# Kernel tuning notes

Hardware: AMD Instinct MI355X
Metric: run time of the kernel (lower is better)

The kernel has to match this reference:

```python
import jax, jax.numpy as jnp
import numpy as np

D_EMB = 256
SCALE = 0.02
B, T = 4, 4096
EPS = 1e-5


def layer_norm(x, w, b):
    m = jnp.mean(x, axis=-1, keepdims=True)
    v = jnp.mean((x - m) ** 2, axis=-1, keepdims=True)
    return (x - m) * jax.lax.rsqrt(v + EPS) * w + b


def setup_inputs() -> dict:
    key = jax.random.key(0)
    ks = jax.random.split(key, 4)
    x = jax.random.normal(ks[0], (B, T, D_EMB), dtype=jnp.float32)
    qkv = jax.random.normal(ks[1], (3, D_EMB, D_EMB), dtype=jnp.float32) * SCALE
    # nn.Linear(D, 2D, bias=False): weight shape (2D, D), applied as x @ W.T
    w1 = jax.random.normal(ks[2], (2 * D_EMB, D_EMB), dtype=jnp.float32) * (1.0 / np.sqrt(D_EMB))
    w2 = jax.random.normal(ks[3], (D_EMB, 2 * D_EMB), dtype=jnp.float32) * (1.0 / np.sqrt(2 * D_EMB))
    ones = jnp.ones((D_EMB,), dtype=jnp.float32)
    zeros = jnp.zeros((D_EMB,), dtype=jnp.float32)
    return {
        "x": x, "qkv": qkv,
        "ln_q_w": ones, "ln_q_b": zeros,
        "ln_k_w": ones, "ln_k_b": zeros,
        "ln_attn_w": ones, "ln_attn_b": zeros,
        "w1": w1, "w2": w2,
        "ln_ff_w": ones, "ln_ff_b": zeros,
    }


def reference(x, qkv, ln_q_w, ln_q_b, ln_k_w, ln_k_b, ln_attn_w, ln_attn_b, w1, w2, ln_ff_w, ln_ff_b):
    # QKV projections: [3, B, T, D]
    y = jnp.einsum('btd,ndD->nbtD', x, qkv)
    q, k, v = y[0], y[1], y[2]
    q = layer_norm(q, ln_q_w, ln_q_b)
    k = layer_norm(k, ln_k_w, ln_k_b)
    # full (non-causal) single-head attention, scale by sqrt(D_EMB)
    scores = jnp.einsum('btd,bsd->bts', q, k) / jnp.sqrt(jnp.float32(D_EMB))
    attn = jax.nn.softmax(scores, axis=-1)
    y = jnp.einsum('bts,bsd->btd', attn, v)
    y = layer_norm(y, ln_attn_w, ln_attn_b)
    x = 0.7 * (x + y)
    # FFN with dual leaky_relu
    y = jax.nn.leaky_relu(x @ w1.T, negative_slope=0.2)
    y = jax.nn.leaky_relu(y @ w2.T, negative_slope=0.2)
    y = layer_norm(y, ln_ff_w, ln_ff_b)
    return 0.7 * (x + y)
```

## Files before the change

### kernel.cpp

```cpp
#include <hip/hip_runtime.h>

#define BSZ   4
#define TSEQ  4096
#define DEMB  256
#define NTOK  (BSZ * TSEQ)
#define HID   512
#define SPLITS 4
#define KEYS_PER_SPLIT (TSEQ / SPLITS)
#define TK 32
#define NT (KEYS_PER_SPLIT / TK)
#define KIMG_STRIDE 8704
#define VIMG_STRIDE 10240

using bf16x8 = __attribute__((ext_vector_type(8))) short;
using f32x16 = __attribute__((ext_vector_type(16))) float;

static __device__ __forceinline__ unsigned short f2bf(float f) {
  union { float f; unsigned u; } v; v.f = f;
  unsigned r = v.u + 0x7FFF + ((v.u >> 16) & 1);
  return (unsigned short)(r >> 16);
}
static __device__ __forceinline__ float bf2f(unsigned short u) {
  union { unsigned u; float f; } v; v.u = ((unsigned)u) << 16;
  return v.f;
}

static __device__ __forceinline__ void async16(void* lds, const void* gp) {
  __builtin_amdgcn_global_load_lds(
      (const __attribute__((address_space(1))) unsigned int*)gp,
      (__attribute__((address_space(3))) unsigned int*)lds, 16, 0, 0);
}

__global__ __launch_bounds__(256) void prep_kernel(
    const float* __restrict__ qkv, const float* __restrict__ w1,
    const float* __restrict__ w2, unsigned short* __restrict__ qkvT,
    unsigned short* __restrict__ w1b, unsigned short* __restrict__ w2b)
{
  const int tid = threadIdx.x;
  if (blockIdx.y < 3) {
    if (blockIdx.x >= 16) return;
    __shared__ float Ts[64][65];
    const int z  = blockIdx.y;
    const int k0 = (blockIdx.x >> 2) * 64;
    const int j0 = (blockIdx.x & 3) * 64;
    const float* src = qkv + (size_t)z * DEMB * DEMB + (size_t)k0 * DEMB + j0;
#pragma unroll
    for (int p = 0; p < 4; ++p) {
      int idx = p * 256 + tid;
      int r = idx >> 4, g = idx & 15;
      float4 v = *(const float4*)(src + (size_t)r * DEMB + g * 4);
      Ts[r][g * 4 + 0] = v.x; Ts[r][g * 4 + 1] = v.y;
      Ts[r][g * 4 + 2] = v.z; Ts[r][g * 4 + 3] = v.w;
    }
    __syncthreads();
    unsigned short* dst = qkvT + (size_t)z * DEMB * DEMB + (size_t)j0 * DEMB + k0;
#pragma unroll
    for (int p = 0; p < 4; ++p) {
      int idx = p * 256 + tid;
      int r = idx >> 4, g = idx & 15;
      ushort4 o;
      o.x = f2bf(Ts[g * 4 + 0][r]); o.y = f2bf(Ts[g * 4 + 1][r]);
      o.z = f2bf(Ts[g * 4 + 2][r]); o.w = f2bf(Ts[g * 4 + 3][r]);
      *(ushort4*)(dst + (size_t)r * DEMB + g * 4) = o;
    }
  } else {
    const float* s = (blockIdx.y == 3) ? w1 : w2;
    unsigned short* d = (blockIdx.y == 3) ? w1b : w2b;
    const int i = blockIdx.x * 256 + tid;
    float4 v = ((const float4*)s)[i];
    ushort4 o;
    o.x = f2bf(v.x); o.y = f2bf(v.y); o.z = f2bf(v.z); o.w = f2bf(v.w);
    ((ushort4*)d)[i] = o;
  }
}

template <int ACT, int MODE, int AF32>
__global__ __launch_bounds__(256, 3) void gemm_bf16_kernel(
    const void* __restrict__ Av, const unsigned short* __restrict__ Bt,
    float* __restrict__ Cf, unsigned short* __restrict__ C0,
    unsigned short* __restrict__ C1, unsigned short* __restrict__ C2,
    int M, int N, int K)
{
  __shared__ __align__(16) unsigned short As[128 * 72];
  __shared__ __align__(16) unsigned short Bs[128 * 72];

  const int tid = threadIdx.x;
  const int w   = tid >> 6;
  const int wm  = w >> 1, wn = w & 1;
  const int l   = tid & 63;
  const int lm  = l & 31;
  const int lh  = l >> 5;

  const int m0    = blockIdx.x * 128;
  const int nbase = blockIdx.y * 128;

  f32x16 acc00, acc01, acc10, acc11;
#pragma unroll
  for (int r = 0; r < 16; ++r) { acc00[r] = 0.f; acc01[r] = 0.f; acc10[r] = 0.f; acc11[r] = 0.f; }

  const int lr = tid >> 3;
  const int lc = (tid & 7) * 8;
  const int fr = tid >> 4;
  const int fc = (tid & 15) * 4;

  const unsigned short* Ab = (const unsigned short*)Av;
  const float* Af = (const float*)Av;

  bf16x8 arb[4], brb[4];
  float4 arf[8];

#pragma unroll
  for (int i = 0; i < (AF32 ? 8 : 4); ++i) {
    if (AF32) arf[i] = *(const float4*)(Af + (size_t)(m0 + i * 16 + fr) * K + fc);
    else      arb[i] = *(const bf16x8*)(Ab + (size_t)(m0 + i * 32 + lr) * K + lc);
  }
#pragma unroll
  for (int i = 0; i < 4; ++i)
    brb[i] = *(const bf16x8*)(Bt + (size_t)(nbase + i * 32 + lr) * K + lc);

  for (int k0 = 0; k0 < K; k0 += 64) {
    __syncthreads();
    if (AF32) {
#pragma unroll
      for (int i = 0; i < 8; ++i) {
        ushort4 u;
        u.x = f2bf(arf[i].x); u.y = f2bf(arf[i].y);
        u.z = f2bf(arf[i].z); u.w = f2bf(arf[i].w);
        *(ushort4*)&As[(i * 16 + fr) * 72 + fc] = u;
      }
    } else {
#pragma unroll
      for (int i = 0; i < 4; ++i) *(bf16x8*)&As[(i * 32 + lr) * 72 + lc] = arb[i];
    }
#pragma unroll
    for (int i = 0; i < 4; ++i) *(bf16x8*)&Bs[(i * 32 + lr) * 72 + lc] = brb[i];
    __syncthreads();

    if (k0 + 64 < K) {
      const int kn = k0 + 64;
#pragma unroll
      for (int i = 0; i < (AF32 ? 8 : 4); ++i) {
        if (AF32) arf[i] = *(const float4*)(Af + (size_t)(m0 + i * 16 + fr) * K + kn + fc);
        else      arb[i] = *(const bf16x8*)(Ab + (size_t)(m0 + i * 32 + lr) * K + kn + lc);
      }
#pragma unroll
      for (int i = 0; i < 4; ++i)
        brb[i] = *(const bf16x8*)(Bt + (size_t)(nbase + i * 32 + lr) * K + kn + lc);
    }

#pragma unroll
    for (int ks = 0; ks < 4; ++ks) {
      bf16x8 a0 = *(const bf16x8*)&As[(wm * 64 + lm)      * 72 + ks * 16 + lh * 8];
      bf16x8 a1 = *(const bf16x8*)&As[(wm * 64 + 32 + lm) * 72 + ks * 16 + lh * 8];
      bf16x8 b0 = *(const bf16x8*)&Bs[(wn * 64 + lm)      * 72 + ks * 16 + lh * 8];
      bf16x8 b1 = *(const bf16x8*)&Bs[(wn * 64 + 32 + lm) * 72 + ks * 16 + lh * 8];
      acc00 = __builtin_amdgcn_mfma_f32_32x32x16_bf16(a0, b0, acc00, 0, 0, 0);
      acc01 = __builtin_amdgcn_mfma_f32_32x32x16_bf16(a0, b1, acc01, 0, 0, 0);
      acc10 = __builtin_amdgcn_mfma_f32_32x32x16_bf16(a1, b0, acc10, 0, 0, 0);
      acc11 = __builtin_amdgcn_mfma_f32_32x32x16_bf16(a1, b1, acc11, 0, 0, 0);
    }
  }

  unsigned short* Cb = C0;
  int col0, ldc;
  if (MODE == 2) {
    const int sel = blockIdx.y >> 1;
    Cb = (sel == 0) ? C0 : (sel == 1 ? C1 : C2);
    col0 = (blockIdx.y & 1) * 128;
    ldc = DEMB;
  } else {
    col0 = nbase;
    ldc = N;
  }
  const f32x16* accs[4] = { &acc00, &acc01, &acc10, &acc11 };
#pragma unroll
  for (int am = 0; am < 2; ++am)
#pragma unroll
    for (int bn = 0; bn < 2; ++bn) {
      const f32x16& a = *accs[am * 2 + bn];
#pragma unroll
      for (int r = 0; r < 16; ++r) {
        const int m = m0 + wm * 64 + am * 32 + (r & 3) + 8 * (r >> 2) + 4 * lh;
        const int n = col0 + wn * 64 + bn * 32 + lm;
        float v = a[r];
        if (ACT == 1) v = v > 0.f ? v : 0.2f * v;
        if (MODE == 0) Cf[(size_t)m * ldc + n] = v;
        else           Cb[(size_t)m * ldc + n] = f2bf(v);
      }
    }
}

__global__ __launch_bounds__(256) void ln_qk_kernel(
    const unsigned short* __restrict__ Qraw, const unsigned short* __restrict__ Kraw,
    const float* __restrict__ qw, const float* __restrict__ qb,
    const float* __restrict__ kw, const float* __restrict__ kb,
    unsigned short* __restrict__ Qbn, unsigned short* __restrict__ Kimg)
{
  const int isK = blockIdx.y;
  const unsigned short* X = isK ? Kraw : Qraw;
  const float* w = isK ? kw : qw;
  const float* b = isK ? kb : qb;
  const int lane = threadIdx.x & 63;
  const size_t row = (size_t)blockIdx.x * 4 + (threadIdx.x >> 6);
  ushort4 u = *(const ushort4*)&X[row * DEMB + lane * 4];
  float x0 = bf2f(u.x), x1 = bf2f(u.y), x2 = bf2f(u.z), x3 = bf2f(u.w);
  float s  = x0 + x1 + x2 + x3;
  float sq = x0 * x0 + x1 * x1 + x2 * x2 + x3 * x3;
#pragma unroll
  for (int o = 32; o > 0; o >>= 1) { s += __shfl_down(s, o); sq += __shfl_down(sq, o); }
  s = __shfl(s, 0); sq = __shfl(sq, 0);
  const float m  = s * (1.f / DEMB);
  const float rs = rsqrtf(sq * (1.f / DEMB) - m * m + 1e-5f);
  const float4 wv = *(const float4*)&w[lane * 4];
  const float4 bv = *(const float4*)&b[lane * 4];
  ushort4 o;
  o.x = f2bf((x0 - m) * rs * wv.x + bv.x);
  o.y = f2bf((x1 - m) * rs * wv.y + bv.y);
  o.z = f2bf((x2 - m) * rs * wv.z + bv.z);
  o.w = f2bf((x3 - m) * rs * wv.w + bv.w);
  if (!isK) {
    *(ushort4*)&Qbn[row * DEMB + lane * 4] = o;
  } else {
    const int bb = (int)(row >> 12);
    const int t  = (int)(row & 4095);
    *(ushort4*)&Kimg[(size_t)(bb * 128 + (t >> 5)) * KIMG_STRIDE + (t & 31) * 264 + lane * 4] = o;
  }
}

__global__ __launch_bounds__(256) void ln_res_bf16_kernel(
    const unsigned short* __restrict__ Y, const float* __restrict__ Xin,
    const float* __restrict__ w, const float* __restrict__ b,
    float* __restrict__ Out)
{
  const int lane = threadIdx.x & 63;
  const size_t row = (size_t)blockIdx.x * 4 + (threadIdx.x >> 6);
  ushort4 u = *(const ushort4*)&Y[row * DEMB + lane * 4];
  float y0 = bf2f(u.x), y1 = bf2f(u.y), y2 = bf2f(u.z), y3 = bf2f(u.w);
  float s  = y0 + y1 + y2 + y3;
  float sq = y0 * y0 + y1 * y1 + y2 * y2 + y3 * y3;
#pragma unroll
  for (int o = 32; o > 0; o >>= 1) { s += __shfl_down(s, o); sq += __shfl_down(sq, o); }
  s = __shfl(s, 0); sq = __shfl(sq, 0);
  const float m  = s * (1.f / DEMB);
  const float rs = rsqrtf(sq * (1.f / DEMB) - m * m + 1e-5f);
  const float4 wv = *(const float4*)&w[lane * 4];
  const float4 bv = *(const float4*)&b[lane * 4];
  const float4 xi = *(const float4*)&Xin[row * DEMB + lane * 4];
  float4 o;
  o.x = 0.7f * (xi.x + (y0 - m) * rs * wv.x + bv.x);
  o.y = 0.7f * (xi.y + (y1 - m) * rs * wv.y + bv.y);
  o.z = 0.7f * (xi.z + (y2 - m) * rs * wv.z + bv.z);
  o.w = 0.7f * (xi.w + (y3 - m) * rs * wv.w + bv.w);
  *(float4*)&Out[row * DEMB + lane * 4] = o;
}

__global__ __launch_bounds__(256) void vtrans_img_kernel(
    const unsigned short* __restrict__ Vraw, unsigned short* __restrict__ Vimg)
{
  __shared__ float Ts[64][65];
  const int tid = threadIdx.x;
  const int t0 = blockIdx.x * 64;
  const int d0 = blockIdx.y * 64;
  const int b  = blockIdx.z;
  const unsigned short* src = Vraw + ((size_t)b * TSEQ + t0) * DEMB + d0;
#pragma unroll
  for (int p = 0; p < 4; ++p) {
    int idx = p * 256 + tid;
    int r = idx >> 4, g = idx & 15;
    ushort4 u = *(const ushort4*)(src + (size_t)r * DEMB + g * 4);
    Ts[r][g * 4 + 0] = bf2f(u.x); Ts[r][g * 4 + 1] = bf2f(u.y);
    Ts[r][g * 4 + 2] = bf2f(u.z); Ts[r][g * 4 + 3] = bf2f(u.w);
  }
  __syncthreads();
#pragma unroll
  for (int p = 0; p < 4; ++p) {
    int idx = p * 256 + tid;
    int r = idx >> 4, g = idx & 15;
    const int t  = t0 + g * 4;
    const int kt = t >> 5, toff = t & 31;
    ushort4 o;
    o.x = f2bf(Ts[g * 4 + 0][r]); o.y = f2bf(Ts[g * 4 + 1][r]);
    o.z = f2bf(Ts[g * 4 + 2][r]); o.w = f2bf(Ts[g * 4 + 3][r]);
    *(ushort4*)(Vimg + (size_t)(b * 128 + kt) * VIMG_STRIDE + (d0 + r) * 40 + toff) = o;
  }
}

__global__ __launch_bounds__(512) void attn_split_kernel(
    const unsigned short* __restrict__ Qb, const unsigned short* __restrict__ Kimg,
    const unsigned short* __restrict__ Vimg, unsigned short* __restrict__ Opart,
    float* __restrict__ lpart)
{
  __shared__ __align__(16) unsigned short Ks[2][KIMG_STRIDE];
  __shared__ __align__(16) unsigned short Vs[3][VIMG_STRIDE];
  __shared__ __align__(16) unsigned short Pb[8 * 32 * 40];

  const int tid = threadIdx.x;
  const int w   = tid >> 6;
  const int l   = tid & 63;
  const int lm  = l & 31;
  const int lh  = l >> 5;

  const int lin = blockIdx.x;
  const int xcd = lin & 7;
  const int idx = lin >> 3;
  const int b     = xcd >> 1;
  const int split = (xcd & 1) * 2 + (idx & 1);
  const int q0    = (idx >> 1) * 256;

  const unsigned short* Qbase  = Qb + (size_t)b * TSEQ * DEMB;
  const unsigned short* Ktiles = Kimg + (size_t)(b * 128 + split * 32) * KIMG_STRIDE;
  const unsigned short* Vtiles = Vimg + (size_t)(b * 128 + split * 32) * VIMG_STRIDE;

  bf16x8 qf[16];
  {
    const unsigned short* qrow = Qbase + (size_t)(q0 + w * 32 + lm) * DEMB + lh * 8;
#pragma unroll
    for (int ks = 0; ks < 16; ++ks) qf[ks] = *(const bf16x8*)(qrow + ks * 16);
  }

  f32x16 o[8];
  float lsum[16], spv[16];
#pragma unroll
  for (int t = 0; t < 8; ++t)
#pragma unroll
    for (int r = 0; r < 16; ++r) o[t][r] = 0.f;
#pragma unroll
  for (int r = 0; r < 16; ++r) lsum[r] = 0.f;

  unsigned short* Pw = &Pb[w * 32 * 40];

#pragma unroll
  for (int i = 0; i < 3; ++i) {
    const int c = w + 8 * i;
    if (c < 17) async16(&Ks[0][c * 512], Ktiles + c * 512 + l * 8);
  }
#pragma unroll
  for (int i = 0; i < 3; ++i) {
    const int c = w + 8 * i;
    if (c < 20) async16(&Vs[0][c * 512], Vtiles + c * 512 + l * 8);
  }

  {
    __syncthreads();
#pragma unroll
    for (int i = 0; i < 3; ++i) {
      const int c = w + 8 * i;
      if (c < 17) async16(&Ks[1][c * 512], Ktiles + (size_t)KIMG_STRIDE + c * 512 + l * 8);
    }
#pragma unroll
    for (int i = 0; i < 3; ++i) {
      const int c = w + 8 * i;
      if (c < 20) async16(&Vs[1][c * 512], Vtiles + (size_t)VIMG_STRIDE + c * 512 + l * 8);
    }
    f32x16 s;
#pragma unroll
    for (int r = 0; r < 16; ++r) s[r] = 0.f;
#pragma unroll
    for (int ks = 0; ks < 16; ++ks) {
      bf16x8 kf = *(const bf16x8*)&Ks[0][lm * 264 + ks * 16 + lh * 8];
      s = __builtin_amdgcn_mfma_f32_32x32x16_bf16(qf[ks], kf, s, 0, 0, 0);
    }
#pragma unroll
    for (int r = 0; r < 16; ++r) spv[r] = s[r];
  }

  int vprev = 0, vcur = 1, vnext = 2;

  for (int st = 1; st < NT; ++st) {
    __syncthreads();

    if (st + 1 < NT) {
      const unsigned short* kn = Ktiles + (size_t)(st + 1) * KIMG_STRIDE;
      const unsigned short* vn = Vtiles + (size_t)(st + 1) * VIMG_STRIDE;
#pragma unroll
      for (int i = 0; i < 3; ++i) {
        const int c = w + 8 * i;
        if (c < 17) async16(&Ks[(st + 1) & 1][c * 512], kn + c * 512 + l * 8);
      }
#pragma unroll
      for (int i = 0; i < 3; ++i) {
        const int c = w + 8 * i;
        if (c < 20) async16(&Vs[vnext][c * 512], vn + c * 512 + l * 8);
      }
    }

#pragma unroll
    for (int r = 0; r < 16; ++r) {
      const float pv = exp2f(spv[r] * 0.09016844335f - 11.541560327f);
      lsum[r] += pv;
      const int row = (r & 3) + ((r >> 2) << 3) + (lh << 2);
      Pw[row * 40 + lm] = f2bf(pv);
    }
    {
      const unsigned short* Vp = &Vs[vprev][0];
#pragma unroll
      for (int ks = 0; ks < 2; ++ks) {
        bf16x8 pf = *(const bf16x8*)&Pw[lm * 40 + ks * 16 + lh * 8];
#pragma unroll
        for (int t = 0; t < 8; ++t) {
          bf16x8 vf = *(const bf16x8*)&Vp[(t * 32 + lm) * 40 + ks * 16 + lh * 8];
          o[t] = __builtin_amdgcn_mfma_f32_32x32x16_bf16(pf, vf, o[t], 0, 0, 0);
        }
      }
    }

    {
      f32x16 s;
#pragma unroll
      for (int r = 0; r < 16; ++r) s[r] = 0.f;
      const unsigned short* Kp = &Ks[st & 1][0];
#pragma unroll
      for (int ks = 0; ks < 16; ++ks) {
        bf16x8 kf = *(const bf16x8*)&Kp[lm * 264 + ks * 16 + lh * 8];
        s = __builtin_amdgcn_mfma_f32_32x32x16_bf16(qf[ks], kf, s, 0, 0, 0);
      }
#pragma unroll
      for (int r = 0; r < 16; ++r) spv[r] = s[r];
    }

    const int tmp = vprev; vprev = vcur; vcur = vnext; vnext = tmp;
  }

#pragma unroll
  for (int r = 0; r < 16; ++r) {
    const float pv = exp2f(spv[r] * 0.09016844335f - 11.541560327f);
    lsum[r] += pv;
    const int row = (r & 3) + ((r >> 2) << 3) + (lh << 2);
    Pw[row * 40 + lm] = f2bf(pv);
  }
  {
    const unsigned short* Vp = &Vs[vprev][0];
#pragma unroll
    for (int ks = 0; ks < 2; ++ks) {
      bf16x8 pf = *(const bf16x8*)&Pw[lm * 40 + ks * 16 + lh * 8];
#pragma unroll
      for (int t = 0; t < 8; ++t) {
        bf16x8 vf = *(const bf16x8*)&Vp[(t * 32 + lm) * 40 + ks * 16 + lh * 8];
        o[t] = __builtin_amdgcn_mfma_f32_32x32x16_bf16(pf, vf, o[t], 0, 0, 0);
      }
    }
  }

#pragma unroll
  for (int r = 0; r < 16; ++r) {
#pragma unroll
    for (int d = 1; d < 32; d <<= 1) lsum[r] += __shfl_xor(lsum[r], d, 64);
  }
  unsigned short* Ob =
      Opart + ((size_t)split * NTOK + (size_t)b * TSEQ + q0 + w * 32) * DEMB;
  float* lb = lpart + (size_t)split * NTOK + (size_t)b * TSEQ + q0 + w * 32;
#pragma unroll
  for (int r = 0; r < 16; ++r) {
    const int row = (r & 3) + ((r >> 2) << 3) + (lh << 2);
#pragma unroll
    for (int t = 0; t < 8; ++t)
      Ob[(size_t)row * DEMB + t * 32 + lm] = f2bf(o[t][r]);
    if (lm == 0) lb[row] = lsum[r];
  }
}

__global__ __launch_bounds__(256) void combine_lnres_kernel(
    const unsigned short* __restrict__ Opart, const float* __restrict__ lpart,
    const float* __restrict__ Xin, const float* __restrict__ w,
    const float* __restrict__ b, float* __restrict__ Out,
    unsigned short* __restrict__ Outb)
{
  const int lane = threadIdx.x & 63;
  const size_t row = (size_t)blockIdx.x * 4 + (threadIdx.x >> 6);
  float4 acc = make_float4(0.f, 0.f, 0.f, 0.f);
  float lt = 0.f;
#pragma unroll
  for (int p = 0; p < SPLITS; ++p) {
    const ushort4 u = *(const ushort4*)&Opart[((size_t)p * NTOK + row) * DEMB + lane * 4];
    acc.x += bf2f(u.x); acc.y += bf2f(u.y);
    acc.z += bf2f(u.z); acc.w += bf2f(u.w);
    lt += lpart[(size_t)p * NTOK + row];
  }
  const float inv = 1.f / lt;
  const float y0 = acc.x * inv, y1 = acc.y * inv, y2 = acc.z * inv, y3 = acc.w * inv;
  float s  = y0 + y1 + y2 + y3;
  float sq = y0 * y0 + y1 * y1 + y2 * y2 + y3 * y3;
#pragma unroll
  for (int o = 32; o > 0; o >>= 1) { s += __shfl_down(s, o); sq += __shfl_down(sq, o); }
  s = __shfl(s, 0); sq = __shfl(sq, 0);
  const float m  = s * (1.f / DEMB);
  const float rs = rsqrtf(sq * (1.f / DEMB) - m * m + 1e-5f);
  const float4 wv = *(const float4*)&w[lane * 4];
  const float4 bv = *(const float4*)&b[lane * 4];
  const float4 xi = *(const float4*)&Xin[row * DEMB + lane * 4];
  float4 o;
  o.x = 0.7f * (xi.x + (y0 - m) * rs * wv.x + bv.x);
  o.y = 0.7f * (xi.y + (y1 - m) * rs * wv.y + bv.y);
  o.z = 0.7f * (xi.z + (y2 - m) * rs * wv.z + bv.z);
  o.w = 0.7f * (xi.w + (y3 - m) * rs * wv.w + bv.w);
  *(float4*)&Out[row * DEMB + lane * 4] = o;
  ushort4 ob;
  ob.x = f2bf(o.x); ob.y = f2bf(o.y); ob.z = f2bf(o.z); ob.w = f2bf(o.w);
  *(ushort4*)&Outb[row * DEMB + lane * 4] = ob;
}

extern "C" void kernel_launch(void* const* d_in, const int* in_sizes, int n_in,
                              void* d_out, int out_size, void* d_ws, size_t ws_size,
                              hipStream_t stream)
{
  (void)in_sizes; (void)n_in; (void)out_size; (void)ws_size;
  const float* x    = (const float*)d_in[0];
  const float* qkv  = (const float*)d_in[1];
  const float* lnqw = (const float*)d_in[2];
  const float* lnqb = (const float*)d_in[3];
  const float* lnkw = (const float*)d_in[4];
  const float* lnkb = (const float*)d_in[5];
  const float* lnaw = (const float*)d_in[6];
  const float* lnab = (const float*)d_in[7];
  const float* w1   = (const float*)d_in[8];
  const float* w2   = (const float*)d_in[9];
  const float* lnfw = (const float*)d_in[10];
  const float* lnfb = (const float*)d_in[11];
  float* out = (float*)d_out;

  char* W = (char*)d_ws;
  const size_t MB = 1 << 20;
  unsigned short* Qraw  = (unsigned short*)(W + 8 * MB);
  unsigned short* Kraw  = (unsigned short*)(W + 16 * MB);
  unsigned short* Vraw  = (unsigned short*)(W + 24 * MB);
  unsigned short* Qbn   = (unsigned short*)(W + 32 * MB);
  unsigned short* Kimg  = (unsigned short*)(W + 40 * MB);
  unsigned short* Vimg  = (unsigned short*)(W + 49 * MB);
  unsigned short* Opart = (unsigned short*)(W + 0);
  float*          lpart = (float*)(W + 61 * MB);
  unsigned short* x1b   = (unsigned short*)(W + 32 * MB);
  unsigned short* H     = (unsigned short*)(W + 40 * MB);
  unsigned short* Y2b   = (unsigned short*)(W + 0);
  unsigned short* qkvT  = (unsigned short*)(W + 60 * MB);
  unsigned short* w1b   = (unsigned short*)(W + 60 * MB + 512 * 1024);
  unsigned short* w2b   = (unsigned short*)(W + 60 * MB + 768 * 1024);

  const dim3 blk(256);

  prep_kernel<<<dim3(128, 5), blk, 0, stream>>>(qkv, w1, w2, qkvT, w1b, w2b);

  gemm_bf16_kernel<0, 2, 1><<<dim3(NTOK / 128, 6), blk, 0, stream>>>(
      x, qkvT, nullptr, Qraw, Kraw, Vraw, NTOK, 3 * DEMB, DEMB);

  ln_qk_kernel<<<dim3(NTOK / 4, 2), blk, 0, stream>>>(
      Qraw, Kraw, lnqw, lnqb, lnkw, lnkb, Qbn, Kimg);
  vtrans_img_kernel<<<dim3(TSEQ / 64, DEMB / 64, BSZ), blk, 0, stream>>>(Vraw, Vimg);

  attn_split_kernel<<<dim3(256), dim3(512), 0, stream>>>(Qbn, Kimg, Vimg, Opart, lpart);
  combine_lnres_kernel<<<NTOK / 4, blk, 0, stream>>>(Opart, lpart, x, lnaw, lnab, out, x1b);

  gemm_bf16_kernel<1, 1, 0><<<dim3(NTOK / 128, HID / 128), blk, 0, stream>>>(
      x1b, w1b, nullptr, H, nullptr, nullptr, NTOK, HID, DEMB);
  gemm_bf16_kernel<1, 1, 0><<<dim3(NTOK / 128, DEMB / 128), blk, 0, stream>>>(
      H, w2b, nullptr, Y2b, nullptr, nullptr, NTOK, DEMB, HID);

  ln_res_bf16_kernel<<<NTOK / 4, blk, 0, stream>>>(Y2b, out, lnfw, lnfb, out);
}
```

Before: 235.5 us.

## Fuse QKV projection with Q/K layernorm and V transpose into one kernel

Replaces the separate QKV GEMM, Q/K layernorm kernel and V transpose kernel with one kernel. Each block computes 256 tokens by the full 256-wide output of one projection, then applies layernorm in registers for Q/K or transposes through shared memory for V. The aim is to remove the raw Q/K/V round trip through global memory and two kernel launches. In exchange the block is larger (512 threads, 128 accumulator floats per thread, occupancy 1), the Q/K stores are scalar rather than vectorised, and the workspace layout is reshuffled.

```diff
diff --git a/kernel.cpp b/kernel.cpp
--- a/kernel.cpp
+++ b/kernel.cpp
@@ -74,12 +74,156 @@
   }
 }
 
-template <int ACT, int MODE, int AF32>
-__global__ __launch_bounds__(256, 3) void gemm_bf16_kernel(
-    const void* __restrict__ Av, const unsigned short* __restrict__ Bt,
-    float* __restrict__ Cf, unsigned short* __restrict__ C0,
-    unsigned short* __restrict__ C1, unsigned short* __restrict__ C2,
-    int M, int N, int K)
+__global__ __launch_bounds__(512, 1) void qkvln_kernel(
+    const float* __restrict__ x, const unsigned short* __restrict__ qkvT,
+    const float* __restrict__ lnqw, const float* __restrict__ lnqb,
+    const float* __restrict__ lnkw, const float* __restrict__ lnkb,
+    unsigned short* __restrict__ Qbn, unsigned short* __restrict__ Kimg,
+    unsigned short* __restrict__ Vimg)
+{
+  __shared__ __align__(16) unsigned short sh[36864];
+  unsigned short* As = sh;
+  unsigned short* Bs = sh + 256 * 72;
+
+  const int tid = threadIdx.x;
+  const int w   = tid >> 6;
+  const int l   = tid & 63;
+  const int lm  = l & 31;
+  const int lh  = l >> 5;
+  const int z   = blockIdx.y;
+  const int m0  = blockIdx.x * 256;
+  const int bb  = m0 >> 12;
+
+  const unsigned short* Bt = qkvT + (size_t)z * DEMB * DEMB;
+
+  f32x16 o[8];
+#pragma unroll
+  for (int t = 0; t < 8; ++t)
+#pragma unroll
+    for (int r = 0; r < 16; ++r) o[t][r] = 0.f;
+
+  const int fr = tid >> 4;
+  const int fc = (tid & 15) * 4;
+
+  float4 arf[8];
+  bf16x8 brb[4];
+
+#pragma unroll
+  for (int i = 0; i < 8; ++i)
+    arf[i] = *(const float4*)(x + (size_t)(m0 + fr + 32 * i) * DEMB + fc);
+#pragma unroll
+  for (int i = 0; i < 4; ++i) {
+    const int c = tid + 512 * i;
+    brb[i] = *(const bf16x8*)(Bt + (size_t)(c >> 3) * DEMB + (c & 7) * 8);
+  }
+
+  for (int k0 = 0; k0 < DEMB; k0 += 64) {
+    __syncthreads();
+#pragma unroll
+    for (int i = 0; i < 8; ++i) {
+      ushort4 u;
+      u.x = f2bf(arf[i].x); u.y = f2bf(arf[i].y);
+      u.z = f2bf(arf[i].z); u.w = f2bf(arf[i].w);
+      *(ushort4*)&As[(fr + 32 * i) * 72 + fc] = u;
+    }
+#pragma unroll
+    for (int i = 0; i < 4; ++i) {
+      const int c = tid + 512 * i;
+      *(bf16x8*)&Bs[(c >> 3) * 72 + (c & 7) * 8] = brb[i];
+    }
+    __syncthreads();
+
+    if (k0 + 64 < DEMB) {
+      const int kn = k0 + 64;
+#pragma unroll
+      for (int i = 0; i < 8; ++i)
+        arf[i] = *(const float4*)(x + (size_t)(m0 + fr + 32 * i) * DEMB + kn + fc);
+#pragma unroll
+      for (int i = 0; i < 4; ++i) {
+        const int c = tid + 512 * i;
+        brb[i] = *(const bf16x8*)(Bt + (size_t)(c >> 3) * DEMB + kn + (c & 7) * 8);
+      }
+    }
+
+#pragma unroll
+    for (int ks = 0; ks < 4; ++ks) {
+      bf16x8 a = *(const bf16x8*)&As[(w * 32 + lm) * 72 + ks * 16 + lh * 8];
+#pragma unroll
+      for (int t = 0; t < 8; ++t) {
+        bf16x8 b = *(const bf16x8*)&Bs[(t * 32 + lm) * 72 + ks * 16 + lh * 8];
+        o[t] = __builtin_amdgcn_mfma_f32_32x32x16_bf16(a, b, o[t], 0, 0, 0);
+      }
+    }
+  }
+
+  __syncthreads();
+
+  if (z < 2) {
+    const float* wp = z ? lnkw : lnqw;
+    const float* bp = z ? lnkb : lnqb;
+    float wc[8], bc[8];
+#pragma unroll
+    for (int t = 0; t < 8; ++t) { wc[t] = wp[t * 32 + lm]; bc[t] = bp[t * 32 + lm]; }
+#pragma unroll
+    for (int r = 0; r < 16; ++r) {
+      float sv = 0.f, sq = 0.f;
+#pragma unroll
+      for (int t = 0; t < 8; ++t) { const float v = o[t][r]; sv += v; sq += v * v; }
+#pragma unroll
+      for (int d = 1; d < 32; d <<= 1) { sv += __shfl_xor(sv, d, 64); sq += __shfl_xor(sq, d, 64); }
+      const float mean = sv * (1.f / DEMB);
+      const float rs = rsqrtf(sq * (1.f / DEMB) - mean * mean + 1e-5f);
+      const int token = m0 + w * 32 + (r & 3) + 8 * (r >> 2) + 4 * lh;
+      if (z == 0) {
+        unsigned short* dst = Qbn + (size_t)token * DEMB;
+#pragma unroll
+        for (int t = 0; t < 8; ++t)
+          dst[t * 32 + lm] = f2bf((o[t][r] - mean) * rs * wc[t] + bc[t]);
+      } else {
+        const int t5 = token & 4095;
+        unsigned short* dst =
+            Kimg + (size_t)(bb * 128 + (t5 >> 5)) * KIMG_STRIDE + (t5 & 31) * 264;
+#pragma unroll
+        for (int t = 0; t < 8; ++t)
+          dst[t * 32 + lm] = f2bf((o[t][r] - mean) * rs * wc[t] + bc[t]);
+      }
+    }
+  } else {
+#pragma unroll
+    for (int h = 0; h < 2; ++h) {
+      if (h) __syncthreads();
+#pragma unroll
+      for (int t2 = 0; t2 < 4; ++t2) {
+        const int t = h * 4 + t2;
+#pragma unroll
+        for (int r = 0; r < 16; ++r) {
+          const int row = w * 32 + (r & 3) + 8 * (r >> 2) + 4 * lh;
+          sh[row * 130 + t2 * 32 + lm] = f2bf(o[t][r]);
+        }
+      }
+      __syncthreads();
+      const int d2 = tid & 127;
+      const int tq = tid >> 7;
+      const int d  = h * 128 + d2;
+#pragma unroll
+      for (int j = 0; j < 16; ++j) {
+        const int tok0 = tq * 64 + j * 4;
+        ushort4 v;
+        v.x = sh[(tok0 + 0) * 130 + d2];
+        v.y = sh[(tok0 + 1) * 130 + d2];
+        v.z = sh[(tok0 + 2) * 130 + d2];
+        v.w = sh[(tok0 + 3) * 130 + d2];
+        const int gtok = m0 + tok0;
+        const int kt = (gtok & 4095) >> 5;
+        *(ushort4*)(Vimg + (size_t)(bb * 128 + kt) * VIMG_STRIDE + d * 40 + (tok0 & 31)) = v;
+      }
+    }
+  }
+}
+
+__global__ __launch_bounds__(256, 3) void gemm_ffn_kernel(
+    const unsigned short* __restrict__ A, const unsigned short* __restrict__ Bt,
+    unsigned short* __restrict__ C, int M, int N, int K)
 {
   __shared__ __align__(16) unsigned short As[128 * 72];
   __shared__ __align__(16) unsigned short Bs[128 * 72];
@@ -100,52 +244,31 @@
 
   const int lr = tid >> 3;
   const int lc = (tid & 7) * 8;
-  const int fr = tid >> 4;
-  const int fc = (tid & 15) * 4;
-
-  const unsigned short* Ab = (const unsigned short*)Av;
-  const float* Af = (const float*)Av;
 
   bf16x8 arb[4], brb[4];
-  float4 arf[8];
-
-#pragma unroll
-  for (int i = 0; i < (AF32 ? 8 : 4); ++i) {
-    if (AF32) arf[i] = *(const float4*)(Af + (size_t)(m0 + i * 16 + fr) * K + fc);
-    else      arb[i] = *(const bf16x8*)(Ab + (size_t)(m0 + i * 32 + lr) * K + lc);
-  }
-#pragma unroll
-  for (int i = 0; i < 4; ++i)
+
+#pragma unroll
+  for (int i = 0; i < 4; ++i) {
+    arb[i] = *(const bf16x8*)(A  + (size_t)(m0 + i * 32 + lr) * K + lc);
     brb[i] = *(const bf16x8*)(Bt + (size_t)(nbase + i * 32 + lr) * K + lc);
+  }
 
   for (int k0 = 0; k0 < K; k0 += 64) {
     __syncthreads();
-    if (AF32) {
-#pragma unroll
-      for (int i = 0; i < 8; ++i) {
-        ushort4 u;
-        u.x = f2bf(arf[i].x); u.y = f2bf(arf[i].y);
-        u.z = f2bf(arf[i].z); u.w = f2bf(arf[i].w);
-        *(ushort4*)&As[(i * 16 + fr) * 72 + fc] = u;
-      }
-    } else {
-#pragma unroll
-      for (int i = 0; i < 4; ++i) *(bf16x8*)&As[(i * 32 + lr) * 72 + lc] = arb[i];
-    }
-#pragma unroll
-    for (int i = 0; i < 4; ++i) *(bf16x8*)&Bs[(i * 32 + lr) * 72 + lc] = brb[i];
+#pragma unroll
+    for (int i = 0; i < 4; ++i) {
+      *(bf16x8*)&As[(i * 32 + lr) * 72 + lc] = arb[i];
+      *(bf16x8*)&Bs[(i * 32 + lr) * 72 + lc] = brb[i];
+    }
     __syncthreads();
 
     if (k0 + 64 < K) {
       const int kn = k0 + 64;
 #pragma unroll
-      for (int i = 0; i < (AF32 ? 8 : 4); ++i) {
-        if (AF32) arf[i] = *(const float4*)(Af + (size_t)(m0 + i * 16 + fr) * K + kn + fc);
-        else      arb[i] = *(const bf16x8*)(Ab + (size_t)(m0 + i * 32 + lr) * K + kn + lc);
-      }
-#pragma unroll
-      for (int i = 0; i < 4; ++i)
+      for (int i = 0; i < 4; ++i) {
+        arb[i] = *(const bf16x8*)(A  + (size_t)(m0 + i * 32 + lr) * K + kn + lc);
         brb[i] = *(const bf16x8*)(Bt + (size_t)(nbase + i * 32 + lr) * K + kn + lc);
+      }
     }
 
 #pragma unroll
@@ -161,17 +284,6 @@
     }
   }
 
-  unsigned short* Cb = C0;
-  int col0, ldc;
-  if (MODE == 2) {
-    const int sel = blockIdx.y >> 1;
-    Cb = (sel == 0) ? C0 : (sel == 1 ? C1 : C2);
-    col0 = (blockIdx.y & 1) * 128;
-    ldc = DEMB;
-  } else {
-    col0 = nbase;
-    ldc = N;
-  }
   const f32x16* accs[4] = { &acc00, &acc01, &acc10, &acc11 };
 #pragma unroll
   for (int am = 0; am < 2; ++am)
@@ -181,50 +293,12 @@
 #pragma unroll
       for (int r = 0; r < 16; ++r) {
         const int m = m0 + wm * 64 + am * 32 + (r & 3) + 8 * (r >> 2) + 4 * lh;
-        const int n = col0 + wn * 64 + bn * 32 + lm;
+        const int n = nbase + wn * 64 + bn * 32 + lm;
         float v = a[r];
-        if (ACT == 1) v = v > 0.f ? v : 0.2f * v;
-        if (MODE == 0) Cf[(size_t)m * ldc + n] = v;
-        else           Cb[(size_t)m * ldc + n] = f2bf(v);
-      }
-    }
-}
-
-__global__ __launch_bounds__(256) void ln_qk_kernel(
-    const unsigned short* __restrict__ Qraw, const unsigned short* __restrict__ Kraw,
-    const float* __restrict__ qw, const float* __restrict__ qb,
-    const float* __restrict__ kw, const float* __restrict__ kb,
-    unsigned short* __restrict__ Qbn, unsigned short* __restrict__ Kimg)
-{
-  const int isK = blockIdx.y;
-  const unsigned short* X = isK ? Kraw : Qraw;
-  const float* w = isK ? kw : qw;
-  const float* b = isK ? kb : qb;
-  const int lane = threadIdx.x & 63;
-  const size_t row = (size_t)blockIdx.x * 4 + (threadIdx.x >> 6);
-  ushort4 u = *(const ushort4*)&X[row * DEMB + lane * 4];
-  float x0 = bf2f(u.x), x1 = bf2f(u.y), x2 = bf2f(u.z), x3 = bf2f(u.w);
-  float s  = x0 + x1 + x2 + x3;
-  float sq = x0 * x0 + x1 * x1 + x2 * x2 + x3 * x3;
-#pragma unroll
-  for (int o = 32; o > 0; o >>= 1) { s += __shfl_down(s, o); sq += __shfl_down(sq, o); }
-  s = __shfl(s, 0); sq = __shfl(sq, 0);
-  const float m  = s * (1.f / DEMB);
-  const float rs = rsqrtf(sq * (1.f / DEMB) - m * m + 1e-5f);
-  const float4 wv = *(const float4*)&w[lane * 4];
-  const float4 bv = *(const float4*)&b[lane * 4];
-  ushort4 o;
-  o.x = f2bf((x0 - m) * rs * wv.x + bv.x);
-  o.y = f2bf((x1 - m) * rs * wv.y + bv.y);
-  o.z = f2bf((x2 - m) * rs * wv.z + bv.z);
-  o.w = f2bf((x3 - m) * rs * wv.w + bv.w);
-  if (!isK) {
-    *(ushort4*)&Qbn[row * DEMB + lane * 4] = o;
-  } else {
-    const int bb = (int)(row >> 12);
-    const int t  = (int)(row & 4095);
-    *(ushort4*)&Kimg[(size_t)(bb * 128 + (t >> 5)) * KIMG_STRIDE + (t & 31) * 264 + lane * 4] = o;
-  }
+        v = v > 0.f ? v : 0.2f * v;
+        C[(size_t)m * N + n] = f2bf(v);
+      }
+    }
 }
 
 __global__ __launch_bounds__(256) void ln_res_bf16_kernel(
@@ -252,37 +326,6 @@
   o.z = 0.7f * (xi.z + (y2 - m) * rs * wv.z + bv.z);
   o.w = 0.7f * (xi.w + (y3 - m) * rs * wv.w + bv.w);
   *(float4*)&Out[row * DEMB + lane * 4] = o;
-}
-
-__global__ __launch_bounds__(256) void vtrans_img_kernel(
-    const unsigned short* __restrict__ Vraw, unsigned short* __restrict__ Vimg)
-{
-  __shared__ float Ts[64][65];
-  const int tid = threadIdx.x;
-  const int t0 = blockIdx.x * 64;
-  const int d0 = blockIdx.y * 64;
-  const int b  = blockIdx.z;
-  const unsigned short* src = Vraw + ((size_t)b * TSEQ + t0) * DEMB + d0;
-#pragma unroll
-  for (int p = 0; p < 4; ++p) {
-    int idx = p * 256 + tid;
-    int r = idx >> 4, g = idx & 15;
-    ushort4 u = *(const ushort4*)(src + (size_t)r * DEMB + g * 4);
-    Ts[r][g * 4 + 0] = bf2f(u.x); Ts[r][g * 4 + 1] = bf2f(u.y);
-    Ts[r][g * 4 + 2] = bf2f(u.z); Ts[r][g * 4 + 3] = bf2f(u.w);
-  }
-  __syncthreads();
-#pragma unroll
-  for (int p = 0; p < 4; ++p) {
-    int idx = p * 256 + tid;
-    int r = idx >> 4, g = idx & 15;
-    const int t  = t0 + g * 4;
-    const int kt = t >> 5, toff = t & 31;
-    ushort4 o;
-    o.x = f2bf(Ts[g * 4 + 0][r]); o.y = f2bf(Ts[g * 4 + 1][r]);
-    o.z = f2bf(Ts[g * 4 + 2][r]); o.w = f2bf(Ts[g * 4 + 3][r]);
-    *(ushort4*)(Vimg + (size_t)(b * 128 + kt) * VIMG_STRIDE + (d0 + r) * 40 + toff) = o;
-  }
 }
 
 __global__ __launch_bounds__(512) void attn_split_kernel(
@@ -520,39 +563,32 @@
 
   char* W = (char*)d_ws;
   const size_t MB = 1 << 20;
-  unsigned short* Qraw  = (unsigned short*)(W + 8 * MB);
-  unsigned short* Kraw  = (unsigned short*)(W + 16 * MB);
-  unsigned short* Vraw  = (unsigned short*)(W + 24 * MB);
-  unsigned short* Qbn   = (unsigned short*)(W + 32 * MB);
-  unsigned short* Kimg  = (unsigned short*)(W + 40 * MB);
-  unsigned short* Vimg  = (unsigned short*)(W + 49 * MB);
-  unsigned short* Opart = (unsigned short*)(W + 0);
-  float*          lpart = (float*)(W + 61 * MB);
-  unsigned short* x1b   = (unsigned short*)(W + 32 * MB);
-  unsigned short* H     = (unsigned short*)(W + 40 * MB);
-  unsigned short* Y2b   = (unsigned short*)(W + 0);
-  unsigned short* qkvT  = (unsigned short*)(W + 60 * MB);
-  unsigned short* w1b   = (unsigned short*)(W + 60 * MB + 512 * 1024);
-  unsigned short* w2b   = (unsigned short*)(W + 60 * MB + 768 * 1024);
+  unsigned short* Qbn   = (unsigned short*)(W + 0);
+  unsigned short* Kimg  = (unsigned short*)(W + 8 * MB);
+  unsigned short* Vimg  = (unsigned short*)(W + 17 * MB);
+  unsigned short* Opart = (unsigned short*)(W + 28 * MB);
+  float*          lpart = (float*)(W + 60 * MB);
+  unsigned short* x1b   = (unsigned short*)(W + 0);
+  unsigned short* H     = (unsigned short*)(W + 8 * MB);
+  unsigned short* Y2b   = (unsigned short*)(W + 28 * MB);
+  unsigned short* qkvT  = (unsigned short*)(W + 60 * MB + 512 * 1024);
+  unsigned short* w1b   = (unsigned short*)(W + 61 * MB);
+  unsigned short* w2b   = (unsigned short*)(W + 61 * MB + 256 * 1024);
 
   const dim3 blk(256);
 
   prep_kernel<<<dim3(128, 5), blk, 0, stream>>>(qkv, w1, w2, qkvT, w1b, w2b);
 
-  gemm_bf16_kernel<0, 2, 1><<<dim3(NTOK / 128, 6), blk, 0, stream>>>(
-      x, qkvT, nullptr, Qraw, Kraw, Vraw, NTOK, 3 * DEMB, DEMB);
-
-  ln_qk_kernel<<<dim3(NTOK / 4, 2), blk, 0, stream>>>(
-      Qraw, Kraw, lnqw, lnqb, lnkw, lnkb, Qbn, Kimg);
-  vtrans_img_kernel<<<dim3(TSEQ / 64, DEMB / 64, BSZ), blk, 0, stream>>>(Vraw, Vimg);
+  qkvln_kernel<<<dim3(NTOK / 256, 3), dim3(512), 0, stream>>>(
+      x, qkvT, lnqw, lnqb, lnkw, lnkb, Qbn, Kimg, Vimg);
 
   attn_split_kernel<<<dim3(256), dim3(512), 0, stream>>>(Qbn, Kimg, Vimg, Opart, lpart);
   combine_lnres_kernel<<<NTOK / 4, blk, 0, stream>>>(Opart, lpart, x, lnaw, lnab, out, x1b);
 
-  gemm_bf16_kernel<1, 1, 0><<<dim3(NTOK / 128, HID / 128), blk, 0, stream>>>(
-      x1b, w1b, nullptr, H, nullptr, nullptr, NTOK, HID, DEMB);
-  gemm_bf16_kernel<1, 1, 0><<<dim3(NTOK / 128, DEMB / 128), blk, 0, stream>>>(
-      H, w2b, nullptr, Y2b, nullptr, nullptr, NTOK, DEMB, HID);
+  gemm_ffn_kernel<<<dim3(NTOK / 128, HID / 128), blk, 0, stream>>>(
+      x1b, w1b, H, NTOK, HID, DEMB);
+  gemm_ffn_kernel<<<dim3(NTOK / 128, DEMB / 128), blk, 0, stream>>>(
+      H, w2b, Y2b, NTOK, DEMB, HID);
 
   ln_res_bf16_kernel<<<NTOK / 4, blk, 0, stream>>>(Y2b, out, lnfw, lnfb, out);
 }
```

Measured after the change: 228.0 us. 1.03x faster.
